# Performance work log

Hardware: AMD Instinct MI355X
Metric: run time of the kernel (lower is better)

The kernel has to match this reference:

```python
import jax, jax.numpy as jnp
import numpy as np

B, N, K, H = 2, 2048, 48, 128
SCALE = 30.0
LN_EPS = 1e-5


def _gather_nodes(nodes, idx):
    # nodes: [B,N,H], idx: [B,N,K] -> [B,N,K,H]
    return nodes[jnp.arange(nodes.shape[0])[:, None, None], idx]


def _ln(x, g, b):
    m = jnp.mean(x, axis=-1, keepdims=True)
    v = jnp.mean(jnp.square(x - m), axis=-1, keepdims=True)
    return (x - m) * jax.lax.rsqrt(v + LN_EPS) * g + b


def _gelu(x):
    return jax.nn.gelu(x, approximate=False)  # torch.nn.GELU default (erf)


def setup_inputs() -> dict:
    key = jax.random.key(0)
    ks = jax.random.split(key, 24)
    d = {}
    d["h_V"] = jax.random.normal(ks[0], (B, N, H), jnp.float32)
    d["h_E"] = jax.random.normal(ks[1], (B, N, K, H), jnp.float32)
    d["E_idx"] = jax.random.randint(ks[2], (B, N, K), 0, N)
    d["mask_V"] = (jax.random.uniform(ks[3], (B, N)) > 0.1).astype(jnp.float32)
    d["mask_attend"] = (jax.random.uniform(ks[4], (B, N, K)) > 0.1).astype(jnp.float32)
    s = 0.05
    # message MLP (node update): W1 in = 3H
    d["W1_w"] = s * jax.random.normal(ks[5], (3 * H, H), jnp.float32)
    d["W1_b"] = jnp.zeros((H,), jnp.float32)
    d["W2_w"] = s * jax.random.normal(ks[6], (H, H), jnp.float32)
    d["W2_b"] = jnp.zeros((H,), jnp.float32)
    d["W3_w"] = s * jax.random.normal(ks[7], (H, H), jnp.float32)
    d["W3_b"] = jnp.zeros((H,), jnp.float32)
    # message MLP (edge update)
    d["W11_w"] = s * jax.random.normal(ks[8], (3 * H, H), jnp.float32)
    d["W11_b"] = jnp.zeros((H,), jnp.float32)
    d["W12_w"] = s * jax.random.normal(ks[9], (H, H), jnp.float32)
    d["W12_b"] = jnp.zeros((H,), jnp.float32)
    d["W13_w"] = s * jax.random.normal(ks[10], (H, H), jnp.float32)
    d["W13_b"] = jnp.zeros((H,), jnp.float32)
    # FFN
    d["Win_w"] = s * jax.random.normal(ks[11], (H, 4 * H), jnp.float32)
    d["Win_b"] = jnp.zeros((4 * H,), jnp.float32)
    d["Wout_w"] = s * jax.random.normal(ks[12], (4 * H, H), jnp.float32)
    d["Wout_b"] = jnp.zeros((H,), jnp.float32)
    # layernorms
    for i, nm in enumerate(["ln1", "ln2", "ln3"]):
        d[nm + "_g"] = jnp.ones((H,), jnp.float32)
        d[nm + "_b"] = jnp.zeros((H,), jnp.float32)
    return d


def reference(h_V, h_E, E_idx, mask_V, mask_attend,
              W1_w, W1_b, W2_w, W2_b, W3_w, W3_b,
              W11_w, W11_b, W12_w, W12_b, W13_w, W13_b,
              Win_w, Win_b, Wout_w, Wout_b,
              ln1_g, ln1_b, ln2_g, ln2_b, ln3_g, ln3_b):
    # --- node message pass ---
    h_EV = jnp.concatenate([
        jnp.broadcast_to(h_V[:, :, None, :], h_E.shape),
        h_E,
        _gather_nodes(h_V, E_idx),
    ], axis=-1)  # [B,N,K,3H]
    h_msg = _gelu(h_EV @ W1_w + W1_b)
    h_msg = _gelu(h_msg @ W2_w + W2_b)
    h_msg = h_msg @ W3_w + W3_b
    h_msg = mask_attend[..., None] * h_msg
    dh = jnp.sum(h_msg, axis=-2) / SCALE  # [B,N,H]
    h_Vn = _ln(h_V + dh, ln1_g, ln1_b)
    # --- FFN ---
    dh = _gelu(h_Vn @ Win_w + Win_b) @ Wout_w + Wout_b
    h_Vn = _ln(h_Vn + dh, ln2_g, ln2_b)
    h_Vn = mask_V[..., None] * h_Vn
    # --- edge update ---
    h_EV2 = jnp.concatenate([
        jnp.broadcast_to(h_Vn[:, :, None, :], h_E.shape),
        h_E,
        _gather_nodes(h_Vn, E_idx),
    ], axis=-1)
    h_msg2 = _gelu(h_EV2 @ W11_w + W11_b)
    h_msg2 = _gelu(h_msg2 @ W12_w + W12_b)
    h_msg2 = h_msg2 @ W13_w + W13_b
    h_En = _ln(h_E + h_msg2, ln3_g, ln3_b)
    return (h_Vn, h_En)
```

## Files before the change

### kernel.cpp

```cpp
#include <hip/hip_runtime.h>
#include <hip/hip_bf16.h>

#define DEVINL __device__ __forceinline__

typedef __attribute__((ext_vector_type(8))) short short8;
typedef __attribute__((ext_vector_type(4))) float f32x4;

DEVINL unsigned short f2bf(float x) {
  __hip_bfloat16 h = __float2bfloat16(x);
  return __builtin_bit_cast(unsigned short, h);
}
DEVINL unsigned int pk2(float lo, float hi) {
  return (unsigned int)f2bf(lo) | ((unsigned int)f2bf(hi) << 16);
}
DEVINL float bf2f(unsigned short h) {
  union { unsigned int u; float f; } c; c.u = ((unsigned int)h) << 16;
  return c.f;
}
DEVINL float gelu_f(float x) {
  const float u = x * x;
  const float y = x * (0.7978845608f + 0.0356774081f * u);
  const float e = __expf(-2.0f * y);
  return x * __builtin_amdgcn_rcpf(1.0f + e);
}
DEVINL f32x4 mfma16(short8 a, short8 b, f32x4 c) {
  return __builtin_amdgcn_mfma_f32_16x16x32_bf16(a, b, c, 0, 0, 0);
}

template<int KSTEPS, int MT, int NT>
DEVINL void gemm_tiles(const unsigned short* Xl, int ldx,
                       const unsigned short* __restrict__ Wp,
                       int lane, int w, f32x4 (&acc)[MT][2])
{
  const int rr = lane & 15;
  const int kg = (lane >> 4) << 3;
  __builtin_amdgcn_s_setprio(1);
  #pragma unroll
  for (int t = 0; t < KSTEPS; ++t) {
    short8 a[MT];
    #pragma unroll
    for (int m = 0; m < MT; ++m)
      a[m] = *(const short8*)(Xl + (m * 16 + rr) * ldx + t * 32 + kg);
    #pragma unroll
    for (int c = 0; c < 2; ++c) {
      short8 bf = *(const short8*)(Wp + ((size_t)(t * NT + (w * 2 + c)) * 64 + lane) * 8);
      #pragma unroll
      for (int m = 0; m < MT; ++m)
        acc[m][c] = mfma16(a[m], bf, acc[m][c]);
    }
  }
  __builtin_amdgcn_s_setprio(0);
}

__global__ __launch_bounds__(256) void k_pack(
    const float* __restrict__ W1w,  const float* __restrict__ W2w,
    const float* __restrict__ W3w,  const float* __restrict__ W11w,
    const float* __restrict__ W12w, const float* __restrict__ W13w,
    const float* __restrict__ Winw, const float* __restrict__ Woutw,
    unsigned short* __restrict__ dst)
{
  const int f = blockIdx.x * 256 + threadIdx.x;
  if (f >= 36864) return;
  const float* src; int row0 = 0, Ncols = 128, NT = 8, lf;
  if (f < 20480) {
    const int seg = f >> 11; lf = f & 2047;
    switch (seg) {
      case 0: src = W1w;  row0 = 0;   break;
      case 1: src = W1w;  row0 = 128; break;
      case 2: src = W1w;  row0 = 256; break;
      case 3: src = W2w;  break;
      case 4: src = W3w;  break;
      case 5: src = W11w; row0 = 0;   break;
      case 6: src = W11w; row0 = 128; break;
      case 7: src = W11w; row0 = 256; break;
      case 8: src = W12w; break;
      default: src = W13w; break;
    }
  } else if (f < 28672) { src = Winw; lf = f - 20480; NT = 32; Ncols = 512; }
  else { src = Woutw; lf = f - 28672; }
  const int l = lf & 63;
  const int g = lf >> 6;
  const int c = g % NT;
  const int t = g / NT;
  const int r0 = row0 + t * 32 + ((l >> 4) << 3);
  const int col = c * 16 + (l & 15);
  short8 vv;
  #pragma unroll
  for (int b = 0; b < 8; ++b)
    vv[b] = (short)f2bf(src[(size_t)(r0 + b) * Ncols + col]);
  *(short8*)(dst + (size_t)f * 8) = vv;
}

__global__ __launch_bounds__(256) void k_pre(
    const float* __restrict__ X,
    const unsigned short* __restrict__ Wtp,
    const unsigned short* __restrict__ Wbp,
    const float* __restrict__ bias,
    float* __restrict__ P1, unsigned short* __restrict__ P3)
{
  __shared__ __align__(16) unsigned short Xs2[16 * 136];
  const int tid = threadIdx.x;
  const int lane = tid & 63;
  const int w = tid >> 6;
  const int rr = lane & 15;
  const int kg = (lane >> 4) << 3;
  const int row0 = blockIdx.x * 16;

  for (int e = tid; e < 512; e += 256) {
    const int r = e >> 5, q = (e & 31) << 2;
    float4 v = *(const float4*)(X + (size_t)(row0 + r) * 128 + q);
    uint2 pk; pk.x = pk2(v.x, v.y); pk.y = pk2(v.z, v.w);
    *(uint2*)(&Xs2[r * 136 + q]) = pk;
  }
  __syncthreads();

  const f32x4 zf = {0.f, 0.f, 0.f, 0.f};
  f32x4 a0[2] = {zf, zf}, a1[2] = {zf, zf};
  #pragma unroll
  for (int t = 0; t < 4; ++t) {
    const short8 a = *(const short8*)(&Xs2[rr * 136 + t * 32 + kg]);
    #pragma unroll
    for (int c = 0; c < 2; ++c) {
      short8 bt = *(const short8*)(Wtp + ((size_t)(t * 8 + (w * 2 + c)) * 64 + lane) * 8);
      a0[c] = mfma16(a, bt, a0[c]);
      short8 bb = *(const short8*)(Wbp + ((size_t)(t * 8 + (w * 2 + c)) * 64 + lane) * 8);
      a1[c] = mfma16(a, bb, a1[c]);
    }
  }
  #pragma unroll
  for (int c = 0; c < 2; ++c) {
    const int col = w * 32 + c * 16 + rr;
    const float b = bias[col];
    #pragma unroll
    for (int r = 0; r < 4; ++r) {
      const int row = row0 + ((lane >> 4) << 2) + r;
      P1[(size_t)row * 128 + col] = a0[c][r] + b;
      P3[(size_t)row * 128 + col] = f2bf(a1[c][r]);
    }
  }
}

template<bool HEB>
__global__ __launch_bounds__(256) void k_node_t(
    const float* __restrict__ hV, const float* __restrict__ hE,
    unsigned short* __restrict__ hEbOut,
    const int* __restrict__ Eidx, const float* __restrict__ maskA,
    const float* __restrict__ P1g, const unsigned short* __restrict__ P3g,
    const unsigned short* __restrict__ Wmidp,
    const unsigned short* __restrict__ W2p, const float* __restrict__ W2b,
    const unsigned short* __restrict__ W3p, const float* __restrict__ W3b,
    const float* __restrict__ ln1g, const float* __restrict__ ln1b,
    float* __restrict__ hVn1)
{
  __shared__ __align__(16) unsigned short Xs[48 * 136];
  __shared__ __align__(16) unsigned short Ms[48 * 136];
  __shared__ float maskv[48];
  __shared__ float dhs[128];
  __shared__ float red[2];

  const int tid = threadIdx.x;
  const int lane = tid & 63;
  const int w = tid >> 6;
  const int rr = lane & 15;
  const int g4 = (lane >> 4) << 2;
  const int bidx = (blockIdx.x & 7) * 512 + (blockIdx.x >> 3);
  const int bbase = bidx & ~2047;

  const float* hErow = hE + (size_t)bidx * 6144;
  const int* idxr = Eidx + (size_t)bidx * 48;

  if (tid < 48) maskv[tid] = maskA[(size_t)bidx * 48 + tid];

  for (int e = tid; e < 1536; e += 256) {
    const int r = e >> 5, q = (e & 31) << 2;
    float4 v = *(const float4*)(hErow + r * 128 + q);
    uint2 pk; pk.x = pk2(v.x, v.y); pk.y = pk2(v.z, v.w);
    *(uint2*)(&Xs[r * 136 + q]) = pk;
    if constexpr (HEB)
      *(uint2*)(hEbOut + (size_t)bidx * 6144 + r * 128 + q) = pk;
  }
  for (int e = tid; e < 768; e += 256) {
    const int r = e >> 4, q = (e & 15) << 3;
    const int j = idxr[r];
    *(short8*)(&Ms[r * 136 + q]) = *(const short8*)(P3g + (size_t)(bbase + j) * 128 + q);
  }
  const float p1c0 = P1g[(size_t)bidx * 128 + w * 32 + rr];
  const float p1c1 = P1g[(size_t)bidx * 128 + w * 32 + 16 + rr];
  __syncthreads();

  f32x4 acc[3][2];
  #pragma unroll
  for (int m = 0; m < 3; ++m)
    #pragma unroll
    for (int c = 0; c < 2; ++c)
      #pragma unroll
      for (int r = 0; r < 4; ++r) {
        const int row = m * 16 + g4 + r;
        const int col = w * 32 + c * 16 + rr;
        acc[m][c][r] = (c ? p1c1 : p1c0) + bf2f(Ms[row * 136 + col]);
      }

  gemm_tiles<4, 3, 8>(Xs, 136, Wmidp, lane, w, acc);
  #pragma unroll
  for (int m = 0; m < 3; ++m)
    #pragma unroll
    for (int c = 0; c < 2; ++c)
      #pragma unroll
      for (int r = 0; r < 4; ++r) {
        const int row = m * 16 + g4 + r;
        Ms[row * 136 + w * 32 + c * 16 + rr] = f2bf(gelu_f(acc[m][c][r]));
      }
  __syncthreads();

  const f32x4 zf = {0.f, 0.f, 0.f, 0.f};
  #pragma unroll
  for (int m = 0; m < 3; ++m) { acc[m][0] = zf; acc[m][1] = zf; }
  gemm_tiles<4, 3, 8>(Ms, 136, W2p, lane, w, acc);
  {
    const float b0 = W2b[w * 32 + rr], b1 = W2b[w * 32 + 16 + rr];
    #pragma unroll
    for (int m = 0; m < 3; ++m)
      #pragma unroll
      for (int c = 0; c < 2; ++c)
        #pragma unroll
        for (int r = 0; r < 4; ++r) {
          const int row = m * 16 + g4 + r;
          Xs[row * 136 + w * 32 + c * 16 + rr] = f2bf(gelu_f(acc[m][c][r] + (c ? b1 : b0)));
        }
  }
  __syncthreads();

  #pragma unroll
  for (int m = 0; m < 3; ++m) { acc[m][0] = zf; acc[m][1] = zf; }
  gemm_tiles<4, 3, 8>(Xs, 136, W3p, lane, w, acc);

  {
    const float b0 = W3b[w * 32 + rr], b1 = W3b[w * 32 + 16 + rr];
    float p0 = 0.f, p1 = 0.f;
    #pragma unroll
    for (int m = 0; m < 3; ++m)
      #pragma unroll
      for (int r = 0; r < 4; ++r) {
        const float mk = maskv[m * 16 + g4 + r];
        p0 += mk * (acc[m][0][r] + b0);
        p1 += mk * (acc[m][1][r] + b1);
      }
    p0 += __shfl_xor(p0, 16); p0 += __shfl_xor(p0, 32);
    p1 += __shfl_xor(p1, 16); p1 += __shfl_xor(p1, 32);
    if (lane < 16) { dhs[w * 32 + lane] = p0; dhs[w * 32 + 16 + lane] = p1; }
  }
  __syncthreads();

  if (tid < 64) {
    const float x0 = hV[(size_t)bidx * 128 + tid]      + dhs[tid]      * (1.0f / 30.0f);
    const float x1 = hV[(size_t)bidx * 128 + 64 + tid] + dhs[tid + 64] * (1.0f / 30.0f);
    float s = x0 + x1, q2 = x0 * x0 + x1 * x1;
    #pragma unroll
    for (int msk = 1; msk < 64; msk <<= 1) {
      s += __shfl_xor(s, msk);
      q2 += __shfl_xor(q2, msk);
    }
    if (tid == 0) {
      const float mean = s * (1.f / 128.f);
      red[0] = mean;
      red[1] = rsqrtf(q2 * (1.f / 128.f) - mean * mean + 1e-5f);
    }
  }
  __syncthreads();
  if (tid < 128) {
    const float x = hV[(size_t)bidx * 128 + tid] + dhs[tid] * (1.0f / 30.0f);
    hVn1[(size_t)bidx * 128 + tid] = (x - red[0]) * red[1] * ln1g[tid] + ln1b[tid];
  }
}

__global__ __launch_bounds__(256) void k_ffn(
    const float* __restrict__ hVn1,
    const unsigned short* __restrict__ Winp, const float* __restrict__ Winb,
    const unsigned short* __restrict__ Woutp, const float* __restrict__ Woutb,
    const float* __restrict__ ln2g, const float* __restrict__ ln2b,
    const float* __restrict__ maskV,
    const unsigned short* __restrict__ W11tp, const unsigned short* __restrict__ W11bp,
    const float* __restrict__ W11b,
    float* __restrict__ outV, float* __restrict__ P1, unsigned short* __restrict__ P3)
{
  __shared__ __align__(16) unsigned short Xs2[16 * 136];
  __shared__ __align__(16) unsigned short Ys[16 * 520];
  __shared__ __align__(16) unsigned short Ts[16 * 136];
  __shared__ float Rs[16 * 128];

  const int tid = threadIdx.x;
  const int lane = tid & 63;
  const int w = tid >> 6;
  const int rr = lane & 15;
  const int kg = (lane >> 4) << 3;
  const int row0 = blockIdx.x * 16;

  for (int e = tid; e < 512; e += 256) {
    const int r = e >> 5, q = (e & 31) << 2;
    float4 v = *(const float4*)(hVn1 + (size_t)(row0 + r) * 128 + q);
    uint2 pk; pk.x = pk2(v.x, v.y); pk.y = pk2(v.z, v.w);
    *(uint2*)(&Xs2[r * 136 + q]) = pk;
  }
  __syncthreads();

  const f32x4 zf = {0.f, 0.f, 0.f, 0.f};
  f32x4 acc1[8];
  #pragma unroll
  for (int c = 0; c < 8; ++c) acc1[c] = zf;
  #pragma unroll
  for (int t = 0; t < 4; ++t) {
    const short8 a = *(const short8*)(&Xs2[rr * 136 + t * 32 + kg]);
    #pragma unroll
    for (int c = 0; c < 8; ++c) {
      const short8 bf = *(const short8*)(Winp + ((size_t)(t * 32 + w * 8 + c) * 64 + lane) * 8);
      acc1[c] = mfma16(a, bf, acc1[c]);
    }
  }
  #pragma unroll
  for (int c = 0; c < 8; ++c) {
    const int col = w * 128 + c * 16 + rr;
    const float bias = Winb[col];
    #pragma unroll
    for (int r = 0; r < 4; ++r) {
      const int row = ((lane >> 4) << 2) + r;
      Ys[row * 520 + col] = f2bf(gelu_f(acc1[c][r] + bias));
    }
  }
  __syncthreads();

  f32x4 acc2[2];
  acc2[0] = zf; acc2[1] = zf;
  #pragma unroll 4
  for (int t = 0; t < 16; ++t) {
    const short8 a = *(const short8*)(&Ys[rr * 520 + t * 32 + kg]);
    #pragma unroll
    for (int c = 0; c < 2; ++c) {
      const short8 bf = *(const short8*)(Woutp + ((size_t)(t * 8 + w * 2 + c) * 64 + lane) * 8);
      acc2[c] = mfma16(a, bf, acc2[c]);
    }
  }
  #pragma unroll
  for (int c = 0; c < 2; ++c) {
    const int col = w * 32 + c * 16 + rr;
    const float bias = Woutb[col];
    #pragma unroll
    for (int r = 0; r < 4; ++r) {
      const int row = ((lane >> 4) << 2) + r;
      Rs[row * 128 + col] = acc2[c][r] + bias + hVn1[(size_t)(row0 + row) * 128 + col];
    }
  }
  __syncthreads();

  const float g0 = ln2g[lane], g1 = ln2g[lane + 64];
  const float be0 = ln2b[lane], be1 = ln2b[lane + 64];
  for (int i = 0; i < 4; ++i) {
    const int row = w * 4 + i;
    const int grow = row0 + row;
    const float x0 = Rs[row * 128 + lane], x1 = Rs[row * 128 + 64 + lane];
    float s = x0 + x1, q2 = x0 * x0 + x1 * x1;
    #pragma unroll
    for (int msk = 1; msk < 64; msk <<= 1) {
      s += __shfl_xor(s, msk);
      q2 += __shfl_xor(q2, msk);
    }
    const float mean = s * (1.f / 128.f);
    const float rstd = rsqrtf(q2 * (1.f / 128.f) - mean * mean + 1e-5f);
    const float mv = maskV[grow];
    const float y0 = ((x0 - mean) * rstd * g0 + be0) * mv;
    const float y1 = ((x1 - mean) * rstd * g1 + be1) * mv;
    outV[(size_t)grow * 128 + lane]      = y0;
    outV[(size_t)grow * 128 + 64 + lane] = y1;
    Ts[row * 136 + lane]      = f2bf(y0);
    Ts[row * 136 + 64 + lane] = f2bf(y1);
  }
  __syncthreads();

  f32x4 a0[2] = {zf, zf}, a1[2] = {zf, zf};
  #pragma unroll
  for (int t = 0; t < 4; ++t) {
    const short8 a = *(const short8*)(&Ts[rr * 136 + t * 32 + kg]);
    #pragma unroll
    for (int c = 0; c < 2; ++c) {
      short8 bt = *(const short8*)(W11tp + ((size_t)(t * 8 + (w * 2 + c)) * 64 + lane) * 8);
      a0[c] = mfma16(a, bt, a0[c]);
      short8 bb = *(const short8*)(W11bp + ((size_t)(t * 8 + (w * 2 + c)) * 64 + lane) * 8);
      a1[c] = mfma16(a, bb, a1[c]);
    }
  }
  #pragma unroll
  for (int c = 0; c < 2; ++c) {
    const int col = w * 32 + c * 16 + rr;
    const float b = W11b[col];
    #pragma unroll
    for (int r = 0; r < 4; ++r) {
      const int row = row0 + ((lane >> 4) << 2) + r;
      P1[(size_t)row * 128 + col] = a0[c][r] + b;
      P3[(size_t)row * 128 + col] = f2bf(a1[c][r]);
    }
  }
}

template<bool HEB>
__global__ __launch_bounds__(256) void k_edge_t(
    const float* __restrict__ hE, const unsigned short* __restrict__ hEb,
    const int* __restrict__ Eidx,
    const float* __restrict__ P1g, const unsigned short* __restrict__ P3g,
    const unsigned short* __restrict__ Wmidp,
    const unsigned short* __restrict__ W12p, const float* __restrict__ W12b,
    const unsigned short* __restrict__ W13p, const float* __restrict__ W13b,
    const float* __restrict__ ln3g, const float* __restrict__ ln3b,
    float* __restrict__ outE)
{
  __shared__ __align__(16) unsigned short Xs[48 * 136];
  __shared__ __align__(16) unsigned short Ms[48 * 136];
  __shared__ float sums[48 * 4];
  __shared__ float sqs[48 * 4];
  __shared__ float mr[96];

  const int tid = threadIdx.x;
  const int lane = tid & 63;
  const int w = tid >> 6;
  const int rr = lane & 15;
  const int g4 = (lane >> 4) << 2;
  const int bidx = (blockIdx.x & 7) * 512 + (blockIdx.x >> 3);
  const int bbase = bidx & ~2047;

  const int* idxr = Eidx + (size_t)bidx * 48;

  if constexpr (HEB) {
    for (int e = tid; e < 768; e += 256) {
      const int r = e >> 4, q = (e & 15) << 3;
      *(short8*)(&Xs[r * 136 + q]) = *(const short8*)(hEb + (size_t)bidx * 6144 + r * 128 + q);
    }
  } else {
    const float* hErow = hE + (size_t)bidx * 6144;
    for (int e = tid; e < 1536; e += 256) {
      const int r = e >> 5, q = (e & 31) << 2;
      float4 v = *(const float4*)(hErow + r * 128 + q);
      uint2 pk; pk.x = pk2(v.x, v.y); pk.y = pk2(v.z, v.w);
      *(uint2*)(&Xs[r * 136 + q]) = pk;
    }
  }
  for (int e = tid; e < 768; e += 256) {
    const int r = e >> 4, q = (e & 15) << 3;
    const int j = idxr[r];
    *(short8*)(&Ms[r * 136 + q]) = *(const short8*)(P3g + (size_t)(bbase + j) * 128 + q);
  }
  const float p1c0 = P1g[(size_t)bidx * 128 + w * 32 + rr];
  const float p1c1 = P1g[(size_t)bidx * 128 + w * 32 + 16 + rr];
  __syncthreads();

  f32x4 acc[3][2];
  float res[3][2][4];
  #pragma unroll
  for (int m = 0; m < 3; ++m)
    #pragma unroll
    for (int c = 0; c < 2; ++c)
      #pragma unroll
      for (int r = 0; r < 4; ++r) {
        const int row = m * 16 + g4 + r;
        const int col = w * 32 + c * 16 + rr;
        acc[m][c][r] = (c ? p1c1 : p1c0) + bf2f(Ms[row * 136 + col]);
        res[m][c][r] = bf2f(Xs[row * 136 + col]);
      }

  gemm_tiles<4, 3, 8>(Xs, 136, Wmidp, lane, w, acc);
  #pragma unroll
  for (int m = 0; m < 3; ++m)
    #pragma unroll
    for (int c = 0; c < 2; ++c)
      #pragma unroll
      for (int r = 0; r < 4; ++r) {
        const int row = m * 16 + g4 + r;
        Ms[row * 136 + w * 32 + c * 16 + rr] = f2bf(gelu_f(acc[m][c][r]));
      }
  __syncthreads();

  const f32x4 zf = {0.f, 0.f, 0.f, 0.f};
  #pragma unroll
  for (int m = 0; m < 3; ++m) { acc[m][0] = zf; acc[m][1] = zf; }
  gemm_tiles<4, 3, 8>(Ms, 136, W12p, lane, w, acc);
  {
    const float b0 = W12b[w * 32 + rr], b1 = W12b[w * 32 + 16 + rr];
    #pragma unroll
    for (int m = 0; m < 3; ++m)
      #pragma unroll
      for (int c = 0; c < 2; ++c)
        #pragma unroll
        for (int r = 0; r < 4; ++r) {
          const int row = m * 16 + g4 + r;
          Xs[row * 136 + w * 32 + c * 16 + rr] = f2bf(gelu_f(acc[m][c][r] + (c ? b1 : b0)));
        }
  }
  __syncthreads();

  #pragma unroll
  for (int m = 0; m < 3; ++m) { acc[m][0] = zf; acc[m][1] = zf; }
  gemm_tiles<4, 3, 8>(Xs, 136, W13p, lane, w, acc);

  {
    const float b0 = W13b[w * 32 + rr], b1 = W13b[w * 32 + 16 + rr];
    #pragma unroll
    for (int m = 0; m < 3; ++m)
      #pragma unroll
      for (int r = 0; r < 4; ++r) {
        const int row = m * 16 + g4 + r;
        acc[m][0][r] += b0 + res[m][0][r];
        acc[m][1][r] += b1 + res[m][1][r];
        float s = acc[m][0][r] + acc[m][1][r];
        float q2 = acc[m][0][r] * acc[m][0][r] + acc[m][1][r] * acc[m][1][r];
        s += __shfl_xor(s, 1); q2 += __shfl_xor(q2, 1);
        s += __shfl_xor(s, 2); q2 += __shfl_xor(q2, 2);
        s += __shfl_xor(s, 4); q2 += __shfl_xor(q2, 4);
        s += __shfl_xor(s, 8); q2 += __shfl_xor(q2, 8);
        if ((lane & 15) == 0) { sums[row * 4 + w] = s; sqs[row * 4 + w] = q2; }
      }
  }
  __syncthreads();
  if (tid < 48) {
    const float s = sums[tid * 4] + sums[tid * 4 + 1] + sums[tid * 4 + 2] + sums[tid * 4 + 3];
    const float q2 = sqs[tid * 4] + sqs[tid * 4 + 1] + sqs[tid * 4 + 2] + sqs[tid * 4 + 3];
    const float mean = s * (1.f / 128.f);
    mr[tid * 2] = mean;
    mr[tid * 2 + 1] = rsqrtf(q2 * (1.f / 128.f) - mean * mean + 1e-5f);
  }
  __syncthreads();
  {
    const float g0 = ln3g[w * 32 + rr], g1 = ln3g[w * 32 + 16 + rr];
    const float be0 = ln3b[w * 32 + rr], be1 = ln3b[w * 32 + 16 + rr];
    #pragma unroll
    for (int m = 0; m < 3; ++m)
      #pragma unroll
      for (int r = 0; r < 4; ++r) {
        const int row = m * 16 + g4 + r;
        const float mean = mr[row * 2], rstd = mr[row * 2 + 1];
        const size_t base = (size_t)bidx * 6144 + (size_t)row * 128 + w * 32 + rr;
        outE[base]      = (acc[m][0][r] - mean) * rstd * g0 + be0;
        outE[base + 16] = (acc[m][1][r] - mean) * rstd * g1 + be1;
      }
  }
}

extern "C" void kernel_launch(void* const* d_in, const int* in_sizes, int n_in,
                              void* d_out, int out_size, void* d_ws, size_t ws_size,
                              hipStream_t stream) {
  const float* hV    = (const float*)d_in[0];
  const float* hE    = (const float*)d_in[1];
  const int*   Eidx  = (const int*)d_in[2];
  const float* maskV = (const float*)d_in[3];
  const float* maskA = (const float*)d_in[4];
  const float* W1w  = (const float*)d_in[5];  const float* W1b  = (const float*)d_in[6];
  const float* W2w  = (const float*)d_in[7];  const float* W2b  = (const float*)d_in[8];
  const float* W3w  = (const float*)d_in[9];  const float* W3b  = (const float*)d_in[10];
  const float* W11w = (const float*)d_in[11]; const float* W11b = (const float*)d_in[12];
  const float* W12w = (const float*)d_in[13]; const float* W12b = (const float*)d_in[14];
  const float* W13w = (const float*)d_in[15]; const float* W13b = (const float*)d_in[16];
  const float* Winw = (const float*)d_in[17]; const float* Winb = (const float*)d_in[18];
  const float* Woutw= (const float*)d_in[19]; const float* Woutb= (const float*)d_in[20];
  const float* ln1g = (const float*)d_in[21]; const float* ln1b = (const float*)d_in[22];
  const float* ln2g = (const float*)d_in[23]; const float* ln2b = (const float*)d_in[24];
  const float* ln3g = (const float*)d_in[25]; const float* ln3b = (const float*)d_in[26];

  float* outV = (float*)d_out;
  float* outE = outV + (size_t)4096 * 128;

  char* ws = (char*)d_ws;
  float* hVn1 = (float*)ws;
  float* P1   = (float*)(ws + (size_t)2 * 1024 * 1024);
  unsigned short* P3 = (unsigned short*)(ws + (size_t)4 * 1024 * 1024);
  unsigned short* Wp = (unsigned short*)(ws + (size_t)5 * 1024 * 1024);
  unsigned short* hEb = (unsigned short*)(ws + (size_t)6 * 1024 * 1024);

  const size_t NEED = (size_t)6 * 1024 * 1024 + (size_t)4096 * 48 * 128 * 2;
  const bool heb = ws_size >= NEED;

  const unsigned short* W1top_p  = Wp;
  const unsigned short* W1mid_p  = Wp + (size_t)2048 * 8;
  const unsigned short* W1bot_p  = Wp + (size_t)4096 * 8;
  const unsigned short* W2p      = Wp + (size_t)6144 * 8;
  const unsigned short* W3p      = Wp + (size_t)8192 * 8;
  const unsigned short* W11top_p = Wp + (size_t)10240 * 8;
  const unsigned short* W11mid_p = Wp + (size_t)12288 * 8;
  const unsigned short* W11bot_p = Wp + (size_t)14336 * 8;
  const unsigned short* W12p     = Wp + (size_t)16384 * 8;
  const unsigned short* W13p     = Wp + (size_t)18432 * 8;
  const unsigned short* Winp     = Wp + (size_t)20480 * 8;
  const unsigned short* Woutp    = Wp + (size_t)28672 * 8;

  k_pack<<<144, 256, 0, stream>>>(W1w, W2w, W3w, W11w, W12w, W13w, Winw, Woutw, Wp);
  k_pre<<<256, 256, 0, stream>>>(hV, W1top_p, W1bot_p, W1b, P1, P3);

  if (heb)
    k_node_t<true><<<4096, 256, 0, stream>>>(hV, hE, hEb, Eidx, maskA, P1, P3,
                                             W1mid_p, W2p, W2b, W3p, W3b,
                                             ln1g, ln1b, hVn1);
  else
    k_node_t<false><<<4096, 256, 0, stream>>>(hV, hE, hEb, Eidx, maskA, P1, P3,
                                              W1mid_p, W2p, W2b, W3p, W3b,
                                              ln1g, ln1b, hVn1);

  k_ffn<<<256, 256, 0, stream>>>(hVn1, Winp, Winb, Woutp, Woutb,
                                 ln2g, ln2b, maskV,
                                 W11top_p, W11bot_p, W11b,
                                 outV, P1, P3);

  if (heb)
    k_edge_t<true><<<4096, 256, 0, stream>>>(hE, hEb, Eidx, P1, P3,
                                             W11mid_p, W12p, W12b, W13p, W13b,
                                             ln3g, ln3b, outE);
  else
    k_edge_t<false><<<4096, 256, 0, stream>>>(hE, hEb, Eidx, P1, P3,
                                              W11mid_p, W12p, W12b, W13p, W13b,
                                              ln3g, ln3b, outE);
}
```

Before: 142.9 us.

## Assign one node per wavefront in node and edge MLP kernels

Restructures the node and edge kernels so each 64-lane wavefront owns a whole node (48 edges x 128 columns) instead of four waves sharing one node. The edge features are loaded from global memory straight into MFMA A-fragments with no LDS staging. Block-level __syncthreads and the cross-wave LayerNorm reductions are replaced by wave-local shuffles, and the grid shrinks to a quarter as many blocks. In exchange each wave holds 96 accumulator registers, which lowers occupancy. The LN3 residual is now re-read from global memory, and the direct A-fragment loads are strided rather than coalesced.

```diff
diff --git a/kernel.cpp b/kernel.cpp
--- a/kernel.cpp
+++ b/kernel.cpp
@@ -25,31 +25,6 @@
 }
 DEVINL f32x4 mfma16(short8 a, short8 b, f32x4 c) {
   return __builtin_amdgcn_mfma_f32_16x16x32_bf16(a, b, c, 0, 0, 0);
-}
-
-template<int KSTEPS, int MT, int NT>
-DEVINL void gemm_tiles(const unsigned short* Xl, int ldx,
-                       const unsigned short* __restrict__ Wp,
-                       int lane, int w, f32x4 (&acc)[MT][2])
-{
-  const int rr = lane & 15;
-  const int kg = (lane >> 4) << 3;
-  __builtin_amdgcn_s_setprio(1);
-  #pragma unroll
-  for (int t = 0; t < KSTEPS; ++t) {
-    short8 a[MT];
-    #pragma unroll
-    for (int m = 0; m < MT; ++m)
-      a[m] = *(const short8*)(Xl + (m * 16 + rr) * ldx + t * 32 + kg);
-    #pragma unroll
-    for (int c = 0; c < 2; ++c) {
-      short8 bf = *(const short8*)(Wp + ((size_t)(t * NT + (w * 2 + c)) * 64 + lane) * 8);
-      #pragma unroll
-      for (int m = 0; m < MT; ++m)
-        acc[m][c] = mfma16(a[m], bf, acc[m][c]);
-    }
-  }
-  __builtin_amdgcn_s_setprio(0);
 }
 
 __global__ __launch_bounds__(256) void k_pack(
@@ -140,10 +115,10 @@
   }
 }
 
-template<bool HEB>
+template<bool HEBW>
 __global__ __launch_bounds__(256) void k_node_t(
     const float* __restrict__ hV, const float* __restrict__ hE,
-    unsigned short* __restrict__ hEbOut,
+    unsigned short* __restrict__ hEb,
     const int* __restrict__ Eidx, const float* __restrict__ maskA,
     const float* __restrict__ P1g, const unsigned short* __restrict__ P3g,
     const unsigned short* __restrict__ Wmidp,
@@ -152,124 +127,170 @@
     const float* __restrict__ ln1g, const float* __restrict__ ln1b,
     float* __restrict__ hVn1)
 {
-  __shared__ __align__(16) unsigned short Xs[48 * 136];
-  __shared__ __align__(16) unsigned short Ms[48 * 136];
-  __shared__ float maskv[48];
-  __shared__ float dhs[128];
-  __shared__ float red[2];
+  __shared__ __align__(16) unsigned short MsAll[4][48 * 136];
 
   const int tid = threadIdx.x;
   const int lane = tid & 63;
-  const int w = tid >> 6;
-  const int rr = lane & 15;
-  const int g4 = (lane >> 4) << 2;
-  const int bidx = (blockIdx.x & 7) * 512 + (blockIdx.x >> 3);
-  const int bbase = bidx & ~2047;
-
-  const float* hErow = hE + (size_t)bidx * 6144;
-  const int* idxr = Eidx + (size_t)bidx * 48;
-
-  if (tid < 48) maskv[tid] = maskA[(size_t)bidx * 48 + tid];
-
-  for (int e = tid; e < 1536; e += 256) {
-    const int r = e >> 5, q = (e & 31) << 2;
-    float4 v = *(const float4*)(hErow + r * 128 + q);
-    uint2 pk; pk.x = pk2(v.x, v.y); pk.y = pk2(v.z, v.w);
-    *(uint2*)(&Xs[r * 136 + q]) = pk;
-    if constexpr (HEB)
-      *(uint2*)(hEbOut + (size_t)bidx * 6144 + r * 128 + q) = pk;
-  }
-  for (int e = tid; e < 768; e += 256) {
+  const int wid = tid >> 6;
+  const int ph = lane & 15;
+  const int q4 = (lane >> 4) << 2;
+  const int kg = (lane >> 4) << 3;
+  const int nb = (blockIdx.x & 7) * 128 + (blockIdx.x >> 3);
+  const int node = nb * 4 + wid;
+  const int bbase = node & ~2047;
+
+  unsigned short* Ms = &MsAll[wid][0];
+  const int* idxr = Eidx + (size_t)node * 48;
+
+  #pragma unroll
+  for (int i = 0; i < 12; ++i) {
+    const int e = i * 64 + lane;
     const int r = e >> 4, q = (e & 15) << 3;
     const int j = idxr[r];
     *(short8*)(&Ms[r * 136 + q]) = *(const short8*)(P3g + (size_t)(bbase + j) * 128 + q);
   }
-  const float p1c0 = P1g[(size_t)bidx * 128 + w * 32 + rr];
-  const float p1c1 = P1g[(size_t)bidx * 128 + w * 32 + 16 + rr];
-  __syncthreads();
-
-  f32x4 acc[3][2];
-  #pragma unroll
-  for (int m = 0; m < 3; ++m)
-    #pragma unroll
-    for (int c = 0; c < 2; ++c)
-      #pragma unroll
-      for (int r = 0; r < 4; ++r) {
-        const int row = m * 16 + g4 + r;
-        const int col = w * 32 + c * 16 + rr;
-        acc[m][c][r] = (c ? p1c1 : p1c0) + bf2f(Ms[row * 136 + col]);
-      }
-
-  gemm_tiles<4, 3, 8>(Xs, 136, Wmidp, lane, w, acc);
-  #pragma unroll
-  for (int m = 0; m < 3; ++m)
-    #pragma unroll
-    for (int c = 0; c < 2; ++c)
-      #pragma unroll
-      for (int r = 0; r < 4; ++r) {
-        const int row = m * 16 + g4 + r;
-        Ms[row * 136 + w * 32 + c * 16 + rr] = f2bf(gelu_f(acc[m][c][r]));
-      }
-  __syncthreads();
-
-  const f32x4 zf = {0.f, 0.f, 0.f, 0.f};
-  #pragma unroll
-  for (int m = 0; m < 3; ++m) { acc[m][0] = zf; acc[m][1] = zf; }
-  gemm_tiles<4, 3, 8>(Ms, 136, W2p, lane, w, acc);
+
+  float p1v[8];
+  #pragma unroll
+  for (int c = 0; c < 8; ++c) p1v[c] = P1g[(size_t)node * 128 + c * 16 + ph];
+  f32x4 acc[3][8];
+  #pragma unroll
+  for (int m = 0; m < 3; ++m)
+    #pragma unroll
+    for (int c = 0; c < 8; ++c)
+      #pragma unroll
+      for (int r = 0; r < 4; ++r)
+        acc[m][c][r] = p1v[c] + bf2f(Ms[(m * 16 + q4 + r) * 136 + c * 16 + ph]);
+
   {
-    const float b0 = W2b[w * 32 + rr], b1 = W2b[w * 32 + 16 + rr];
+    const float* Arow = hE + (size_t)node * 6144;
+    unsigned short* Hrow = hEb + (size_t)node * 6144;
+    #pragma unroll
+    for (int t = 0; t < 4; ++t) {
+      short8 a[3];
+      #pragma unroll
+      for (int m = 0; m < 3; ++m) {
+        const float* p = Arow + (m * 16 + ph) * 128 + t * 32 + kg;
+        float4 v0 = *(const float4*)p;
+        float4 v1 = *(const float4*)(p + 4);
+        uint4 pk;
+        pk.x = pk2(v0.x, v0.y); pk.y = pk2(v0.z, v0.w);
+        pk.z = pk2(v1.x, v1.y); pk.w = pk2(v1.z, v1.w);
+        if constexpr (HEBW)
+          *(uint4*)(Hrow + (m * 16 + ph) * 128 + t * 32 + kg) = pk;
+        a[m] = __builtin_bit_cast(short8, pk);
+      }
+      #pragma unroll
+      for (int c = 0; c < 8; ++c) {
+        const short8 bf = *(const short8*)(Wmidp + ((size_t)(t * 8 + c) * 64 + lane) * 8);
+        #pragma unroll
+        for (int m = 0; m < 3; ++m)
+          acc[m][c] = mfma16(a[m], bf, acc[m][c]);
+      }
+    }
+  }
+  #pragma unroll
+  for (int m = 0; m < 3; ++m)
+    #pragma unroll
+    for (int c = 0; c < 8; ++c)
+      #pragma unroll
+      for (int r = 0; r < 4; ++r)
+        Ms[(m * 16 + q4 + r) * 136 + c * 16 + ph] = f2bf(gelu_f(acc[m][c][r]));
+
+  {
+    float b2v[8];
+    #pragma unroll
+    for (int c = 0; c < 8; ++c) b2v[c] = W2b[c * 16 + ph];
     #pragma unroll
     for (int m = 0; m < 3; ++m)
       #pragma unroll
-      for (int c = 0; c < 2; ++c)
+      for (int c = 0; c < 8; ++c)
+        acc[m][c] = (f32x4){b2v[c], b2v[c], b2v[c], b2v[c]};
+    #pragma unroll
+    for (int t = 0; t < 4; ++t) {
+      short8 a[3];
+      #pragma unroll
+      for (int m = 0; m < 3; ++m)
+        a[m] = *(const short8*)(&Ms[(m * 16 + ph) * 136 + t * 32 + kg]);
+      #pragma unroll
+      for (int c = 0; c < 8; ++c) {
+        const short8 bf = *(const short8*)(W2p + ((size_t)(t * 8 + c) * 64 + lane) * 8);
         #pragma unroll
-        for (int r = 0; r < 4; ++r) {
-          const int row = m * 16 + g4 + r;
-          Xs[row * 136 + w * 32 + c * 16 + rr] = f2bf(gelu_f(acc[m][c][r] + (c ? b1 : b0)));
-        }
-  }
-  __syncthreads();
-
-  #pragma unroll
-  for (int m = 0; m < 3; ++m) { acc[m][0] = zf; acc[m][1] = zf; }
-  gemm_tiles<4, 3, 8>(Xs, 136, W3p, lane, w, acc);
+        for (int m = 0; m < 3; ++m)
+          acc[m][c] = mfma16(a[m], bf, acc[m][c]);
+      }
+    }
+  }
+  #pragma unroll
+  for (int m = 0; m < 3; ++m)
+    #pragma unroll
+    for (int c = 0; c < 8; ++c)
+      #pragma unroll
+      for (int r = 0; r < 4; ++r)
+        Ms[(m * 16 + q4 + r) * 136 + c * 16 + ph] = f2bf(gelu_f(acc[m][c][r]));
 
   {
-    const float b0 = W3b[w * 32 + rr], b1 = W3b[w * 32 + 16 + rr];
-    float p0 = 0.f, p1 = 0.f;
+    float b3v[8];
+    #pragma unroll
+    for (int c = 0; c < 8; ++c) b3v[c] = W3b[c * 16 + ph];
     #pragma unroll
     for (int m = 0; m < 3; ++m)
       #pragma unroll
-      for (int r = 0; r < 4; ++r) {
-        const float mk = maskv[m * 16 + g4 + r];
-        p0 += mk * (acc[m][0][r] + b0);
-        p1 += mk * (acc[m][1][r] + b1);
-      }
-    p0 += __shfl_xor(p0, 16); p0 += __shfl_xor(p0, 32);
-    p1 += __shfl_xor(p1, 16); p1 += __shfl_xor(p1, 32);
-    if (lane < 16) { dhs[w * 32 + lane] = p0; dhs[w * 32 + 16 + lane] = p1; }
-  }
-  __syncthreads();
-
-  if (tid < 64) {
-    const float x0 = hV[(size_t)bidx * 128 + tid]      + dhs[tid]      * (1.0f / 30.0f);
-    const float x1 = hV[(size_t)bidx * 128 + 64 + tid] + dhs[tid + 64] * (1.0f / 30.0f);
-    float s = x0 + x1, q2 = x0 * x0 + x1 * x1;
-    #pragma unroll
-    for (int msk = 1; msk < 64; msk <<= 1) {
-      s += __shfl_xor(s, msk);
-      q2 += __shfl_xor(q2, msk);
-    }
-    if (tid == 0) {
-      const float mean = s * (1.f / 128.f);
-      red[0] = mean;
-      red[1] = rsqrtf(q2 * (1.f / 128.f) - mean * mean + 1e-5f);
-    }
-  }
-  __syncthreads();
-  if (tid < 128) {
-    const float x = hV[(size_t)bidx * 128 + tid] + dhs[tid] * (1.0f / 30.0f);
-    hVn1[(size_t)bidx * 128 + tid] = (x - red[0]) * red[1] * ln1g[tid] + ln1b[tid];
+      for (int c = 0; c < 8; ++c)
+        acc[m][c] = (f32x4){b3v[c], b3v[c], b3v[c], b3v[c]};
+    #pragma unroll
+    for (int t = 0; t < 4; ++t) {
+      short8 a[3];
+      #pragma unroll
+      for (int m = 0; m < 3; ++m)
+        a[m] = *(const short8*)(&Ms[(m * 16 + ph) * 136 + t * 32 + kg]);
+      #pragma unroll
+      for (int c = 0; c < 8; ++c) {
+        const short8 bf = *(const short8*)(W3p + ((size_t)(t * 8 + c) * 64 + lane) * 8);
+        #pragma unroll
+        for (int m = 0; m < 3; ++m)
+          acc[m][c] = mfma16(a[m], bf, acc[m][c]);
+      }
+    }
+  }
+
+  float p[8];
+  #pragma unroll
+  for (int c = 0; c < 8; ++c) p[c] = 0.f;
+  #pragma unroll
+  for (int m = 0; m < 3; ++m)
+    #pragma unroll
+    for (int r = 0; r < 4; ++r) {
+      const float mk = maskA[(size_t)node * 48 + m * 16 + q4 + r];
+      #pragma unroll
+      for (int c = 0; c < 8; ++c) p[c] += mk * acc[m][c][r];
+    }
+  #pragma unroll
+  for (int c = 0; c < 8; ++c) {
+    p[c] += __shfl_xor(p[c], 16);
+    p[c] += __shfl_xor(p[c], 32);
+  }
+  float x[8];
+  float s = 0.f, sq = 0.f;
+  #pragma unroll
+  for (int c = 0; c < 8; ++c) {
+    x[c] = hV[(size_t)node * 128 + c * 16 + ph] + p[c] * (1.0f / 30.0f);
+    s += x[c]; sq += x[c] * x[c];
+  }
+  #pragma unroll
+  for (int msk = 1; msk <= 8; msk <<= 1) {
+    s += __shfl_xor(s, msk);
+    sq += __shfl_xor(sq, msk);
+  }
+  const float mean = s * (1.f / 128.f);
+  const float rstd = rsqrtf(sq * (1.f / 128.f) - mean * mean + 1e-5f);
+  const int c0 = (lane >> 4) * 2;
+  #pragma unroll
+  for (int cc = 0; cc < 2; ++cc) {
+    const int c = c0 + cc;
+    const int col = c * 16 + ph;
+    hVn1[(size_t)node * 128 + col] =
+        (x[c] - mean) * rstd * ln1g[col] + ln1b[col];
   }
 }
 
@@ -411,134 +432,164 @@
     const float* __restrict__ ln3g, const float* __restrict__ ln3b,
     float* __restrict__ outE)
 {
-  __shared__ __align__(16) unsigned short Xs[48 * 136];
-  __shared__ __align__(16) unsigned short Ms[48 * 136];
-  __shared__ float sums[48 * 4];
-  __shared__ float sqs[48 * 4];
-  __shared__ float mr[96];
+  __shared__ __align__(16) unsigned short MsAll[4][48 * 136];
 
   const int tid = threadIdx.x;
   const int lane = tid & 63;
-  const int w = tid >> 6;
-  const int rr = lane & 15;
-  const int g4 = (lane >> 4) << 2;
-  const int bidx = (blockIdx.x & 7) * 512 + (blockIdx.x >> 3);
-  const int bbase = bidx & ~2047;
-
-  const int* idxr = Eidx + (size_t)bidx * 48;
-
-  if constexpr (HEB) {
-    for (int e = tid; e < 768; e += 256) {
-      const int r = e >> 4, q = (e & 15) << 3;
-      *(short8*)(&Xs[r * 136 + q]) = *(const short8*)(hEb + (size_t)bidx * 6144 + r * 128 + q);
-    }
-  } else {
-    const float* hErow = hE + (size_t)bidx * 6144;
-    for (int e = tid; e < 1536; e += 256) {
-      const int r = e >> 5, q = (e & 31) << 2;
-      float4 v = *(const float4*)(hErow + r * 128 + q);
-      uint2 pk; pk.x = pk2(v.x, v.y); pk.y = pk2(v.z, v.w);
-      *(uint2*)(&Xs[r * 136 + q]) = pk;
-    }
-  }
-  for (int e = tid; e < 768; e += 256) {
+  const int wid = tid >> 6;
+  const int ph = lane & 15;
+  const int q4 = (lane >> 4) << 2;
+  const int kg = (lane >> 4) << 3;
+  const int nb = (blockIdx.x & 7) * 128 + (blockIdx.x >> 3);
+  const int node = nb * 4 + wid;
+  const int bbase = node & ~2047;
+
+  unsigned short* Ms = &MsAll[wid][0];
+  const int* idxr = Eidx + (size_t)node * 48;
+
+  #pragma unroll
+  for (int i = 0; i < 12; ++i) {
+    const int e = i * 64 + lane;
     const int r = e >> 4, q = (e & 15) << 3;
     const int j = idxr[r];
     *(short8*)(&Ms[r * 136 + q]) = *(const short8*)(P3g + (size_t)(bbase + j) * 128 + q);
   }
-  const float p1c0 = P1g[(size_t)bidx * 128 + w * 32 + rr];
-  const float p1c1 = P1g[(size_t)bidx * 128 + w * 32 + 16 + rr];
-  __syncthreads();
-
-  f32x4 acc[3][2];
-  float res[3][2][4];
-  #pragma unroll
-  for (int m = 0; m < 3; ++m)
-    #pragma unroll
-    for (int c = 0; c < 2; ++c)
-      #pragma unroll
-      for (int r = 0; r < 4; ++r) {
-        const int row = m * 16 + g4 + r;
-        const int col = w * 32 + c * 16 + rr;
-        acc[m][c][r] = (c ? p1c1 : p1c0) + bf2f(Ms[row * 136 + col]);
-        res[m][c][r] = bf2f(Xs[row * 136 + col]);
-      }
-
-  gemm_tiles<4, 3, 8>(Xs, 136, Wmidp, lane, w, acc);
-  #pragma unroll
-  for (int m = 0; m < 3; ++m)
-    #pragma unroll
-    for (int c = 0; c < 2; ++c)
-      #pragma unroll
-      for (int r = 0; r < 4; ++r) {
-        const int row = m * 16 + g4 + r;
-        Ms[row * 136 + w * 32 + c * 16 + rr] = f2bf(gelu_f(acc[m][c][r]));
-      }
-  __syncthreads();
-
-  const f32x4 zf = {0.f, 0.f, 0.f, 0.f};
-  #pragma unroll
-  for (int m = 0; m < 3; ++m) { acc[m][0] = zf; acc[m][1] = zf; }
-  gemm_tiles<4, 3, 8>(Ms, 136, W12p, lane, w, acc);
+
+  float p1v[8];
+  #pragma unroll
+  for (int c = 0; c < 8; ++c) p1v[c] = P1g[(size_t)node * 128 + c * 16 + ph];
+  f32x4 acc[3][8];
+  #pragma unroll
+  for (int m = 0; m < 3; ++m)
+    #pragma unroll
+    for (int c = 0; c < 8; ++c)
+      #pragma unroll
+      for (int r = 0; r < 4; ++r)
+        acc[m][c][r] = p1v[c] + bf2f(Ms[(m * 16 + q4 + r) * 136 + c * 16 + ph]);
+
+  #pragma unroll
+  for (int t = 0; t < 4; ++t) {
+    short8 a[3];
+    #pragma unroll
+    for (int m = 0; m < 3; ++m) {
+      if constexpr (HEB) {
+        a[m] = *(const short8*)(hEb + (size_t)node * 6144 + (m * 16 + ph) * 128 + t * 32 + kg);
+      } else {
+        const float* p = hE + (size_t)node * 6144 + (m * 16 + ph) * 128 + t * 32 + kg;
+        float4 v0 = *(const float4*)p;
+        float4 v1 = *(const float4*)(p + 4);
+        uint4 pk;
+        pk.x = pk2(v0.x, v0.y); pk.y = pk2(v0.z, v0.w);
+        pk.z = pk2(v1.x, v1.y); pk.w = pk2(v1.z, v1.w);
+        a[m] = __builtin_bit_cast(short8, pk);
+      }
+    }
+    #pragma unroll
+    for (int c = 0; c < 8; ++c) {
+      const short8 bf = *(const short8*)(Wmidp + ((size_t)(t * 8 + c) * 64 + lane) * 8);
+      #pragma unroll
+      for (int m = 0; m < 3; ++m)
+        acc[m][c] = mfma16(a[m], bf, acc[m][c]);
+    }
+  }
+  #pragma unroll
+  for (int m = 0; m < 3; ++m)
+    #pragma unroll
+    for (int c = 0; c < 8; ++c)
+      #pragma unroll
+      for (int r = 0; r < 4; ++r)
+        Ms[(m * 16 + q4 + r) * 136 + c * 16 + ph] = f2bf(gelu_f(acc[m][c][r]));
+
   {
-    const float b0 = W12b[w * 32 + rr], b1 = W12b[w * 32 + 16 + rr];
+    float b2v[8];
+    #pragma unroll
+    for (int c = 0; c < 8; ++c) b2v[c] = W12b[c * 16 + ph];
     #pragma unroll
     for (int m = 0; m < 3; ++m)
       #pragma unroll
-      for (int c = 0; c < 2; ++c)
+      for (int c = 0; c < 8; ++c)
+        acc[m][c] = (f32x4){b2v[c], b2v[c], b2v[c], b2v[c]};
+    #pragma unroll
+    for (int t = 0; t < 4; ++t) {
+      short8 a[3];
+      #pragma unroll
+      for (int m = 0; m < 3; ++m)
+        a[m] = *(const short8*)(&Ms[(m * 16 + ph) * 136 + t * 32 + kg]);
+      #pragma unroll
+      for (int c = 0; c < 8; ++c) {
+        const short8 bf = *(const short8*)(W12p + ((size_t)(t * 8 + c) * 64 + lane) * 8);
         #pragma unroll
-        for (int r = 0; r < 4; ++r) {
-          const int row = m * 16 + g4 + r;
-          Xs[row * 136 + w * 32 + c * 16 + rr] = f2bf(gelu_f(acc[m][c][r] + (c ? b1 : b0)));
-        }
-  }
-  __syncthreads();
-
-  #pragma unroll
-  for (int m = 0; m < 3; ++m) { acc[m][0] = zf; acc[m][1] = zf; }
-  gemm_tiles<4, 3, 8>(Xs, 136, W13p, lane, w, acc);
+        for (int m = 0; m < 3; ++m)
+          acc[m][c] = mfma16(a[m], bf, acc[m][c]);
+      }
+    }
+  }
+  #pragma unroll
+  for (int m = 0; m < 3; ++m)
+    #pragma unroll
+    for (int c = 0; c < 8; ++c)
+      #pragma unroll
+      for (int r = 0; r < 4; ++r)
+        Ms[(m * 16 + q4 + r) * 136 + c * 16 + ph] = f2bf(gelu_f(acc[m][c][r]));
 
   {
-    const float b0 = W13b[w * 32 + rr], b1 = W13b[w * 32 + 16 + rr];
+    float b3v[8];
+    #pragma unroll
+    for (int c = 0; c < 8; ++c) b3v[c] = W13b[c * 16 + ph];
     #pragma unroll
     for (int m = 0; m < 3; ++m)
       #pragma unroll
-      for (int r = 0; r < 4; ++r) {
-        const int row = m * 16 + g4 + r;
-        acc[m][0][r] += b0 + res[m][0][r];
-        acc[m][1][r] += b1 + res[m][1][r];
-        float s = acc[m][0][r] + acc[m][1][r];
-        float q2 = acc[m][0][r] * acc[m][0][r] + acc[m][1][r] * acc[m][1][r];
-        s += __shfl_xor(s, 1); q2 += __shfl_xor(q2, 1);
-        s += __shfl_xor(s, 2); q2 += __shfl_xor(q2, 2);
-        s += __shfl_xor(s, 4); q2 += __shfl_xor(q2, 4);
-        s += __shfl_xor(s, 8); q2 += __shfl_xor(q2, 8);
-        if ((lane & 15) == 0) { sums[row * 4 + w] = s; sqs[row * 4 + w] = q2; }
-      }
-  }
-  __syncthreads();
-  if (tid < 48) {
-    const float s = sums[tid * 4] + sums[tid * 4 + 1] + sums[tid * 4 + 2] + sums[tid * 4 + 3];
-    const float q2 = sqs[tid * 4] + sqs[tid * 4 + 1] + sqs[tid * 4 + 2] + sqs[tid * 4 + 3];
-    const float mean = s * (1.f / 128.f);
-    mr[tid * 2] = mean;
-    mr[tid * 2 + 1] = rsqrtf(q2 * (1.f / 128.f) - mean * mean + 1e-5f);
-  }
-  __syncthreads();
-  {
-    const float g0 = ln3g[w * 32 + rr], g1 = ln3g[w * 32 + 16 + rr];
-    const float be0 = ln3b[w * 32 + rr], be1 = ln3b[w * 32 + 16 + rr];
-    #pragma unroll
-    for (int m = 0; m < 3; ++m)
-      #pragma unroll
-      for (int r = 0; r < 4; ++r) {
-        const int row = m * 16 + g4 + r;
-        const float mean = mr[row * 2], rstd = mr[row * 2 + 1];
-        const size_t base = (size_t)bidx * 6144 + (size_t)row * 128 + w * 32 + rr;
-        outE[base]      = (acc[m][0][r] - mean) * rstd * g0 + be0;
-        outE[base + 16] = (acc[m][1][r] - mean) * rstd * g1 + be1;
-      }
-  }
+      for (int c = 0; c < 8; ++c)
+        acc[m][c] = (f32x4){b3v[c], b3v[c], b3v[c], b3v[c]};
+    #pragma unroll
+    for (int t = 0; t < 4; ++t) {
+      short8 a[3];
+      #pragma unroll
+      for (int m = 0; m < 3; ++m)
+        a[m] = *(const short8*)(&Ms[(m * 16 + ph) * 136 + t * 32 + kg]);
+      #pragma unroll
+      for (int c = 0; c < 8; ++c) {
+        const short8 bf = *(const short8*)(W13p + ((size_t)(t * 8 + c) * 64 + lane) * 8);
+        #pragma unroll
+        for (int m = 0; m < 3; ++m)
+          acc[m][c] = mfma16(a[m], bf, acc[m][c]);
+      }
+    }
+  }
+
+  const float lg[8] = {ln3g[ph], ln3g[16 + ph], ln3g[32 + ph], ln3g[48 + ph],
+                       ln3g[64 + ph], ln3g[80 + ph], ln3g[96 + ph], ln3g[112 + ph]};
+  const float lb[8] = {ln3b[ph], ln3b[16 + ph], ln3b[32 + ph], ln3b[48 + ph],
+                       ln3b[64 + ph], ln3b[80 + ph], ln3b[96 + ph], ln3b[112 + ph]};
+  #pragma unroll
+  for (int m = 0; m < 3; ++m)
+    #pragma unroll
+    for (int r = 0; r < 4; ++r) {
+      const int row = m * 16 + q4 + r;
+      float s = 0.f, sq = 0.f;
+      #pragma unroll
+      for (int c = 0; c < 8; ++c) {
+        float res;
+        if constexpr (HEB)
+          res = bf2f(hEb[(size_t)node * 6144 + row * 128 + c * 16 + ph]);
+        else
+          res = hE[(size_t)node * 6144 + row * 128 + c * 16 + ph];
+        acc[m][c][r] += res;
+        s += acc[m][c][r];
+        sq += acc[m][c][r] * acc[m][c][r];
+      }
+      #pragma unroll
+      for (int msk = 1; msk <= 8; msk <<= 1) {
+        s += __shfl_xor(s, msk);
+        sq += __shfl_xor(sq, msk);
+      }
+      const float mean = s * (1.f / 128.f);
+      const float rstd = rsqrtf(sq * (1.f / 128.f) - mean * mean + 1e-5f);
+      #pragma unroll
+      for (int c = 0; c < 8; ++c)
+        outE[(size_t)node * 6144 + row * 128 + c * 16 + ph] =
+            (acc[m][c][r] - mean) * rstd * lg[c] + lb[c];
+    }
 }
 
 extern "C" void kernel_launch(void* const* d_in, const int* in_sizes, int n_in,
@@ -591,11 +642,11 @@
   k_pre<<<256, 256, 0, stream>>>(hV, W1top_p, W1bot_p, W1b, P1, P3);
 
   if (heb)
-    k_node_t<true><<<4096, 256, 0, stream>>>(hV, hE, hEb, Eidx, maskA, P1, P3,
+    k_node_t<true><<<1024, 256, 0, stream>>>(hV, hE, hEb, Eidx, maskA, P1, P3,
                                              W1mid_p, W2p, W2b, W3p, W3b,
                                              ln1g, ln1b, hVn1);
   else
-    k_node_t<false><<<4096, 256, 0, stream>>>(hV, hE, hEb, Eidx, maskA, P1, P3,
+    k_node_t<false><<<1024, 256, 0, stream>>>(hV, hE, hEb, Eidx, maskA, P1, P3,
                                               W1mid_p, W2p, W2b, W3p, W3b,
                                               ln1g, ln1b, hVn1);
 
@@ -605,11 +656,11 @@
                                  outV, P1, P3);
 
   if (heb)
-    k_edge_t<true><<<4096, 256, 0, stream>>>(hE, hEb, Eidx, P1, P3,
+    k_edge_t<true><<<1024, 256, 0, stream>>>(hE, hEb, Eidx, P1, P3,
                                              W11mid_p, W12p, W12b, W13p, W13b,
                                              ln3g, ln3b, outE);
   else
-    k_edge_t<false><<<4096, 256, 0, stream>>>(hE, hEb, Eidx, P1, P3,
+    k_edge_t<false><<<1024, 256, 0, stream>>>(hE, hEb, Eidx, P1, P3,
                                               W11mid_p, W12p, W12b, W13p, W13b,
                                               ln3g, ln3b, outE);
 }
```

Result: slower. 271.5 us (+90.0%).
